# Performance work log

Hardware: AMD Instinct MI355X
Metric: run time of the kernel (lower is better)

The kernel has to match this reference:

```python
import jax, jax.numpy as jnp
import numpy as np

N_NODES = 50000
N_EDGES = 800000
IN_F = 64
D_ATT = 64
HEADS = 8
D_HEAD = D_ATT // HEADS  # 8


def segment_softmax(logits, seg, num_segments):
    # logits: [E, d]; seg: [E] int segment ids
    m = jax.ops.segment_max(logits, seg, num_segments=num_segments)  # [N, d]
    m = jnp.where(jnp.isfinite(m), m, 0.0)  # guard empty segments
    e = jnp.exp(logits - m[seg])
    s = jax.ops.segment_sum(e, seg, num_segments=num_segments)  # [N, d]
    return e / (s[seg] + 1e-16)


def setup_inputs() -> dict:
    key = jax.random.key(0)
    ks = jax.random.split(key, 8)
    x = jax.random.normal(ks[0], (N_NODES, IN_F), dtype=jnp.float32)
    edge = jax.random.randint(ks[1], (2, N_EDGES), 0, N_NODES, dtype=jnp.int32)
    sc = 1.0 / np.sqrt(IN_F).astype(np.float32)
    Wq = jax.random.normal(ks[2], (IN_F, D_ATT), dtype=jnp.float32) * sc
    Wk = jax.random.normal(ks[3], (IN_F, D_ATT), dtype=jnp.float32) * sc
    Wv = jax.random.normal(ks[4], (IN_F, D_ATT), dtype=jnp.float32) * sc
    bq = jnp.zeros((D_ATT,), jnp.float32)
    bk = jnp.zeros((D_ATT,), jnp.float32)
    bv = jnp.zeros((D_ATT,), jnp.float32)
    return {"x": x, "Wq": Wq, "bq": bq, "Wk": Wk, "bk": bk, "Wv": Wv, "bv": bv, "edge": edge}


def reference(x, Wq, bq, Wk, bk, Wv, bv, edge):
    # Linear projections then split heads: [N, H, D_HEAD]
    q = (x @ Wq + bq).reshape(-1, HEADS, D_HEAD)
    k = (x @ Wk + bk).reshape(-1, HEADS, D_HEAD)
    v = (x @ Wv + bv).reshape(-1, HEADS, D_HEAD)
    src = q[edge[0]]      # [E, H, D_HEAD]
    dst_k = k[edge[1]]    # [E, H, D_HEAD]
    # Faithful to source: sum over dim=1 (the HEAD axis) -> [E, D_HEAD]
    prods = jnp.sum(src * dst_k, axis=1) / np.float32(np.sqrt(D_HEAD))
    # segment softmax grouped by edge[attention_norm_idx] (= edge[1])
    attention = segment_softmax(prods, edge[1], N_NODES)
    return attention, v, prods
```

## Files before the change

kernel.cpp:

```cpp
#include <hip/hip_runtime.h>
#include <hip/hip_bf16.h>

#define N_NODES 50000
#define N_EDGES 800000

typedef __attribute__((ext_vector_type(4))) unsigned int uint4v;

static __device__ __forceinline__ float bfu_lo(unsigned int u) {
    union { unsigned int u; float f; } v; v.u = u << 16; return v.f;
}
static __device__ __forceinline__ float bfu_hi(unsigned int u) {
    union { unsigned int u; float f; } v; v.u = u & 0xffff0000u; return v.f;
}
static __device__ __forceinline__ unsigned short f2bf(float f) {
    union { float f; unsigned int u; } v; v.f = f;
    v.u += 0x7fffu + ((v.u >> 16) & 1u);
    return (unsigned short)(v.u >> 16);
}

__global__ __launch_bounds__(256, 4)
void proj_kernel(const float* __restrict__ x,
                 const float* __restrict__ Wq, const float* __restrict__ bq,
                 const float* __restrict__ Wk, const float* __restrict__ bk,
                 const float* __restrict__ Wv, const float* __restrict__ bv,
                 unsigned short* __restrict__ Qb, unsigned short* __restrict__ Kb,
                 float* __restrict__ V)
{
    __shared__ float xs[64 * 64];
    const int tid  = threadIdx.x;
    const int c    = tid & 63;
    const int w    = tid >> 6;
    const int m    = blockIdx.y;
    const int row0 = blockIdx.x * 64;
    const int nrows = min(64, N_NODES - row0);

    const float* W = (m == 0) ? Wq : (m == 1) ? Wk : Wv;
    const float* b = (m == 0) ? bq : (m == 1) ? bk : bv;
    const int oc = (m == 2) ? c : ((c & 7) * 8 + (c >> 3));
    unsigned short* outb = (m == 0) ? Qb : Kb;

    {
        const float4* xg  = (const float4*)(x + (size_t)row0 * 64);
        float4*       xs4 = (float4*)xs;
        const int nf4 = nrows * 16;
        for (int i = tid; i < nf4; i += 256) xs4[i] = xg[i];
    }
    __syncthreads();

    const float bc = b[c];
    const int r0 = w * 16;

    float acc[16];
#pragma unroll
    for (int i = 0; i < 16; ++i) acc[i] = bc;

    for (int jc = 0; jc < 4; ++jc) {
        float wr[16];
#pragma unroll
        for (int j = 0; j < 16; ++j) wr[j] = W[(jc * 16 + j) * 64 + c];
#pragma unroll
        for (int i = 0; i < 16; ++i) {
            const float4* xr = (const float4*)(xs + (r0 + i) * 64 + jc * 16);
#pragma unroll
            for (int j4 = 0; j4 < 4; ++j4) {
                const float4 xv = xr[j4];
                acc[i] += xv.x * wr[4 * j4 + 0];
                acc[i] += xv.y * wr[4 * j4 + 1];
                acc[i] += xv.z * wr[4 * j4 + 2];
                acc[i] += xv.w * wr[4 * j4 + 3];
            }
        }
    }

#pragma unroll
    for (int i = 0; i < 16; ++i) {
        const int r = r0 + i;
        if (r < nrows) {
            const size_t o = (size_t)(row0 + r) * 64 + oc;
            if (m == 2) V[o] = acc[i];
            else        outb[o] = f2bf(acc[i]);
        }
    }
}

__global__ __launch_bounds__(256)
void edge_kernel(const unsigned short* __restrict__ Qb,
                 const unsigned short* __restrict__ Kb,
                 const int* __restrict__ edge,
                 float* __restrict__ prods, float* __restrict__ ssum)
{
    const int gid = blockIdx.x * 256 + threadIdx.x;
    if (gid >= N_EDGES * 8) return;
    const int e = gid >> 3;
    const int d = gid & 7;
    const int e0 = edge[e];
    const int e1 = edge[N_EDGES + e];

    const uint4v qv = *(const uint4v*)(Qb + (size_t)e0 * 64 + d * 8);
    const uint4v kv = *(const uint4v*)(Kb + (size_t)e1 * 64 + d * 8);
    float s = 0.f;
#pragma unroll
    for (int i = 0; i < 4; ++i) {
        s += bfu_lo(qv[i]) * bfu_lo(kv[i]);
        s += bfu_hi(qv[i]) * bfu_hi(kv[i]);
    }

    const float p = s * 0.35355339059327373f;
    prods[gid] = p;
    atomicAdd(ssum + (size_t)e1 * 8 + d, __expf(p));
}

__global__ __launch_bounds__(256)
void norm_kernel(const int* __restrict__ edge,
                 const float* __restrict__ prods,
                 const float* __restrict__ ssum, float* __restrict__ att)
{
    const int gid = blockIdx.x * 256 + threadIdx.x;
    if (gid >= N_EDGES * 8) return;
    const int e = gid >> 3;
    const int d = gid & 7;
    const int e1 = edge[N_EDGES + e];
    const float ex = __expf(prods[gid]);
    att[gid] = ex / (ssum[(size_t)e1 * 8 + d] + 1e-16f);
}

extern "C" void kernel_launch(void* const* d_in, const int* in_sizes, int n_in,
                              void* d_out, int out_size, void* d_ws, size_t ws_size,
                              hipStream_t stream)
{
    const float* x    = (const float*)d_in[0];
    const float* Wq   = (const float*)d_in[1];
    const float* bq   = (const float*)d_in[2];
    const float* Wk   = (const float*)d_in[3];
    const float* bk   = (const float*)d_in[4];
    const float* Wv   = (const float*)d_in[5];
    const float* bv   = (const float*)d_in[6];
    const int*   edge = (const int*)d_in[7];

    float* out   = (float*)d_out;
    float* att   = out;
    float* V     = out + 6400000;
    float* prods = out + 9600000;

    unsigned short* Qb = (unsigned short*)d_ws;
    unsigned short* Kb = Qb + 3200000;
    float*          ssum = (float*)(Kb + 3200000);

    hipMemsetAsync(ssum, 0, 400000 * sizeof(float), stream);

    dim3 pgrid((N_NODES + 63) / 64, 3);
    proj_kernel<<<pgrid, 256, 0, stream>>>(x, Wq, bq, Wk, bk, Wv, bv,
                                           Qb, Kb, V);

    const int nwork = N_EDGES * 8;
    edge_kernel<<<(nwork + 255) / 256, 256, 0, stream>>>(Qb, Kb, edge, prods,
                                                         ssum);
    norm_kernel<<<(nwork + 255) / 256, 256, 0, stream>>>(edge, prods, ssum,
                                                         att);
}
```

Before: 185.9 us.

## Fuse QKV projections into one pass and merge edge/norm via cooperative grid

```diff
diff --git a/kernel.cpp b/kernel.cpp
--- a/kernel.cpp
+++ b/kernel.cpp
@@ -1,8 +1,13 @@
 #include <hip/hip_runtime.h>
 #include <hip/hip_bf16.h>
+#include <hip/hip_cooperative_groups.h>
+
+namespace cg = cooperative_groups;
 
 #define N_NODES 50000
 #define N_EDGES 800000
+
+#define FUSED_THREADS (1024 * 256)
 
 typedef __attribute__((ext_vector_type(4))) unsigned int uint4v;
 
@@ -18,26 +23,20 @@
     return (unsigned short)(v.u >> 16);
 }
 
-__global__ __launch_bounds__(256, 4)
-void proj_kernel(const float* __restrict__ x,
-                 const float* __restrict__ Wq, const float* __restrict__ bq,
-                 const float* __restrict__ Wk, const float* __restrict__ bk,
-                 const float* __restrict__ Wv, const float* __restrict__ bv,
-                 unsigned short* __restrict__ Qb, unsigned short* __restrict__ Kb,
-                 float* __restrict__ V)
+__global__ __launch_bounds__(256, 2)
+void proj_qkv(const float* __restrict__ x,
+              const float* __restrict__ Wq, const float* __restrict__ bq,
+              const float* __restrict__ Wk, const float* __restrict__ bk,
+              const float* __restrict__ Wv, const float* __restrict__ bv,
+              unsigned short* __restrict__ Qb, unsigned short* __restrict__ Kb,
+              float* __restrict__ V)
 {
     __shared__ float xs[64 * 64];
     const int tid  = threadIdx.x;
     const int c    = tid & 63;
     const int w    = tid >> 6;
-    const int m    = blockIdx.y;
     const int row0 = blockIdx.x * 64;
     const int nrows = min(64, N_NODES - row0);
-
-    const float* W = (m == 0) ? Wq : (m == 1) ? Wk : Wv;
-    const float* b = (m == 0) ? bq : (m == 1) ? bk : bv;
-    const int oc = (m == 2) ? c : ((c & 7) * 8 + (c >> 3));
-    unsigned short* outb = (m == 0) ? Qb : Kb;
 
     {
         const float4* xg  = (const float4*)(x + (size_t)row0 * 64);
@@ -47,27 +46,36 @@
     }
     __syncthreads();
 
-    const float bc = b[c];
+    const float* Ws[3] = {Wq, Wk, Wv};
+    const float* bs[3] = {bq, bk, bv};
     const int r0 = w * 16;
+    const int ocqk = (c & 7) * 8 + (c >> 3);
 
-    float acc[16];
+    float acc[3][16];
 #pragma unroll
-    for (int i = 0; i < 16; ++i) acc[i] = bc;
+    for (int m = 0; m < 3; ++m) {
+        const float bc = bs[m][c];
+#pragma unroll
+        for (int i = 0; i < 16; ++i) acc[m][i] = bc;
+    }
 
     for (int jc = 0; jc < 4; ++jc) {
-        float wr[16];
 #pragma unroll
-        for (int j = 0; j < 16; ++j) wr[j] = W[(jc * 16 + j) * 64 + c];
+        for (int m = 0; m < 3; ++m) {
+            float wr[16];
 #pragma unroll
-        for (int i = 0; i < 16; ++i) {
-            const float4* xr = (const float4*)(xs + (r0 + i) * 64 + jc * 16);
+            for (int j = 0; j < 16; ++j) wr[j] = Ws[m][(jc * 16 + j) * 64 + c];
 #pragma unroll
-            for (int j4 = 0; j4 < 4; ++j4) {
-                const float4 xv = xr[j4];
-                acc[i] += xv.x * wr[4 * j4 + 0];
-                acc[i] += xv.y * wr[4 * j4 + 1];
-                acc[i] += xv.z * wr[4 * j4 + 2];
-                acc[i] += xv.w * wr[4 * j4 + 3];
+            for (int i = 0; i < 16; ++i) {
+                const float4* xr = (const float4*)(xs + (r0 + i) * 64 + jc * 16);
+#pragma unroll
+                for (int j4 = 0; j4 < 4; ++j4) {
+                    const float4 xv = xr[j4];
+                    acc[m][i] += xv.x * wr[4 * j4 + 0];
+                    acc[m][i] += xv.y * wr[4 * j4 + 1];
+                    acc[m][i] += xv.z * wr[4 * j4 + 2];
+                    acc[m][i] += xv.w * wr[4 * j4 + 3];
+                }
             }
         }
     }
@@ -76,52 +84,60 @@
     for (int i = 0; i < 16; ++i) {
         const int r = r0 + i;
         if (r < nrows) {
-            const size_t o = (size_t)(row0 + r) * 64 + oc;
-            if (m == 2) V[o] = acc[i];
-            else        outb[o] = f2bf(acc[i]);
+            const size_t o = (size_t)(row0 + r) * 64;
+            Qb[o + ocqk] = f2bf(acc[0][i]);
+            Kb[o + ocqk] = f2bf(acc[1][i]);
+            __builtin_nontemporal_store(acc[2][i], V + o + c);
         }
     }
 }
 
-__global__ __launch_bounds__(256)
-void edge_kernel(const unsigned short* __restrict__ Qb,
-                 const unsigned short* __restrict__ Kb,
-                 const int* __restrict__ edge,
-                 float* __restrict__ prods, float* __restrict__ ssum)
+__global__ __launch_bounds__(256, 4)
+void edge_fused(const unsigned short* __restrict__ Qb,
+                const unsigned short* __restrict__ Kb,
+                const int* __restrict__ edge,
+                float* __restrict__ prods, float* __restrict__ att,
+                float* __restrict__ ssum)
 {
-    const int gid = blockIdx.x * 256 + threadIdx.x;
-    if (gid >= N_EDGES * 8) return;
-    const int e = gid >> 3;
-    const int d = gid & 7;
-    const int e0 = edge[e];
-    const int e1 = edge[N_EDGES + e];
+    const int tid0 = blockIdx.x * 256 + threadIdx.x;
 
-    const uint4v qv = *(const uint4v*)(Qb + (size_t)e0 * 64 + d * 8);
-    const uint4v kv = *(const uint4v*)(Kb + (size_t)e1 * 64 + d * 8);
-    float s = 0.f;
+    for (int i = tid0; i < N_NODES * 8; i += FUSED_THREADS)
+        __hip_atomic_store(ssum + i, 0.f, __ATOMIC_RELAXED,
+                           __HIP_MEMORY_SCOPE_AGENT);
+    __threadfence();
+    cg::this_grid().sync();
+
+    for (int gid = tid0; gid < N_EDGES * 8; gid += FUSED_THREADS) {
+        const int e = gid >> 3;
+        const int d = gid & 7;
+        const int e0 = edge[e];
+        const int e1 = edge[N_EDGES + e];
+
+        const uint4v qv = *(const uint4v*)(Qb + (size_t)e0 * 64 + d * 8);
+        const uint4v kv = *(const uint4v*)(Kb + (size_t)e1 * 64 + d * 8);
+        float s = 0.f;
 #pragma unroll
-    for (int i = 0; i < 4; ++i) {
-        s += bfu_lo(qv[i]) * bfu_lo(kv[i]);
-        s += bfu_hi(qv[i]) * bfu_hi(kv[i]);
+        for (int i = 0; i < 4; ++i) {
+            s += bfu_lo(qv[i]) * bfu_lo(kv[i]);
+            s += bfu_hi(qv[i]) * bfu_hi(kv[i]);
+        }
+        const float p = s * 0.35355339059327373f;
+        prods[gid] = p;
+        atomicAdd(ssum + (size_t)e1 * 8 + d, __expf(p));
     }
+    __threadfence();
+    cg::this_grid().sync();
 
-    const float p = s * 0.35355339059327373f;
-    prods[gid] = p;
-    atomicAdd(ssum + (size_t)e1 * 8 + d, __expf(p));
-}
-
-__global__ __launch_bounds__(256)
-void norm_kernel(const int* __restrict__ edge,
-                 const float* __restrict__ prods,
-                 const float* __restrict__ ssum, float* __restrict__ att)
-{
-    const int gid = blockIdx.x * 256 + threadIdx.x;
-    if (gid >= N_EDGES * 8) return;
-    const int e = gid >> 3;
-    const int d = gid & 7;
-    const int e1 = edge[N_EDGES + e];
-    const float ex = __expf(prods[gid]);
-    att[gid] = ex / (ssum[(size_t)e1 * 8 + d] + 1e-16f);
+    for (int gid = tid0; gid < N_EDGES * 8; gid += FUSED_THREADS) {
+        const int e = gid >> 3;
+        const int d = gid & 7;
+        const int e1 = edge[N_EDGES + e];
+        const float p = prods[gid];
+        const float s = __hip_atomic_load(ssum + (size_t)e1 * 8 + d,
+                                          __ATOMIC_RELAXED,
+                                          __HIP_MEMORY_SCOPE_AGENT);
+        __builtin_nontemporal_store(__expf(p) / (s + 1e-16f), att + gid);
+    }
 }
 
 extern "C" void kernel_launch(void* const* d_in, const int* in_sizes, int n_in,
@@ -146,15 +162,11 @@
     unsigned short* Kb = Qb + 3200000;
     float*          ssum = (float*)(Kb + 3200000);
 
-    hipMemsetAsync(ssum, 0, 400000 * sizeof(float), stream);
+    proj_qkv<<<(N_NODES + 63) / 64, 256, 0, stream>>>(x, Wq, bq, Wk, bk,
+                                                      Wv, bv, Qb, Kb, V);
 
-    dim3 pgrid((N_NODES + 63) / 64, 3);
-    proj_kernel<<<pgrid, 256, 0, stream>>>(x, Wq, bq, Wk, bk, Wv, bv,
-                                           Qb, Kb, V);
-
-    const int nwork = N_EDGES * 8;
-    edge_kernel<<<(nwork + 255) / 256, 256, 0, stream>>>(Qb, Kb, edge, prods,
-                                                         ssum);
-    norm_kernel<<<(nwork + 255) / 256, 256, 0, stream>>>(edge, prods, ssum,
-                                                         att);
+    void* args[] = {(void*)&Qb, (void*)&Kb, (void*)&edge,
+                    (void*)&prods, (void*)&att, (void*)&ssum};
+    hipLaunchCooperativeKernel((void*)edge_fused, dim3(1024), dim3(256),
+                               args, 0, stream);
 }
```

New measurement: 573.7 us. 209% more time.

## Fuse QKV projections into one kernel and fold ssum zeroing in

Applied to the files above, without the earlier changes.

```diff
diff --git a/kernel.cpp b/kernel.cpp
--- a/kernel.cpp
+++ b/kernel.cpp
@@ -18,26 +18,25 @@
     return (unsigned short)(v.u >> 16);
 }
 
-__global__ __launch_bounds__(256, 4)
-void proj_kernel(const float* __restrict__ x,
-                 const float* __restrict__ Wq, const float* __restrict__ bq,
-                 const float* __restrict__ Wk, const float* __restrict__ bk,
-                 const float* __restrict__ Wv, const float* __restrict__ bv,
-                 unsigned short* __restrict__ Qb, unsigned short* __restrict__ Kb,
-                 float* __restrict__ V)
+__global__ __launch_bounds__(256, 2)
+void proj_qkv(const float* __restrict__ x,
+              const float* __restrict__ Wq, const float* __restrict__ bq,
+              const float* __restrict__ Wk, const float* __restrict__ bk,
+              const float* __restrict__ Wv, const float* __restrict__ bv,
+              unsigned short* __restrict__ Qb, unsigned short* __restrict__ Kb,
+              float* __restrict__ V, float* __restrict__ ssum)
 {
-    __shared__ float xs[64 * 64];
+    __shared__ float xs[32 * 64];
     const int tid  = threadIdx.x;
     const int c    = tid & 63;
     const int w    = tid >> 6;
-    const int m    = blockIdx.y;
-    const int row0 = blockIdx.x * 64;
-    const int nrows = min(64, N_NODES - row0);
+    const int row0 = blockIdx.x * 32;
+    const int nrows = min(32, N_NODES - row0);
 
-    const float* W = (m == 0) ? Wq : (m == 1) ? Wk : Wv;
-    const float* b = (m == 0) ? bq : (m == 1) ? bk : bv;
-    const int oc = (m == 2) ? c : ((c & 7) * 8 + (c >> 3));
-    unsigned short* outb = (m == 0) ? Qb : Kb;
+    {
+        const int z = blockIdx.x * 256 + tid;
+        if (z < N_NODES * 8) ssum[z] = 0.f;
+    }
 
     {
         const float4* xg  = (const float4*)(x + (size_t)row0 * 64);
@@ -47,38 +46,44 @@
     }
     __syncthreads();
 
-    const float bc = b[c];
-    const int r0 = w * 16;
+    const int r0 = w * 8;
 
-    float acc[16];
+    float accq[8], acck[8], accv[8];
+    {
+        const float bqc = bq[c], bkc = bk[c], bvc = bv[c];
 #pragma unroll
-    for (int i = 0; i < 16; ++i) acc[i] = bc;
+        for (int i = 0; i < 8; ++i) { accq[i] = bqc; acck[i] = bkc; accv[i] = bvc; }
+    }
 
-    for (int jc = 0; jc < 4; ++jc) {
-        float wr[16];
+    for (int jc = 0; jc < 8; ++jc) {
+        float wq[8], wk[8], wv[8];
 #pragma unroll
-        for (int j = 0; j < 16; ++j) wr[j] = W[(jc * 16 + j) * 64 + c];
+        for (int j = 0; j < 8; ++j) {
+            const int row = (jc * 8 + j) * 64 + c;
+            wq[j] = Wq[row]; wk[j] = Wk[row]; wv[j] = Wv[row];
+        }
 #pragma unroll
-        for (int i = 0; i < 16; ++i) {
-            const float4* xr = (const float4*)(xs + (r0 + i) * 64 + jc * 16);
-#pragma unroll
-            for (int j4 = 0; j4 < 4; ++j4) {
-                const float4 xv = xr[j4];
-                acc[i] += xv.x * wr[4 * j4 + 0];
-                acc[i] += xv.y * wr[4 * j4 + 1];
-                acc[i] += xv.z * wr[4 * j4 + 2];
-                acc[i] += xv.w * wr[4 * j4 + 3];
-            }
+        for (int i = 0; i < 8; ++i) {
+            const float4* xr = (const float4*)(xs + (r0 + i) * 64 + jc * 8);
+            const float4 xv0 = xr[0], xv1 = xr[1];
+            accq[i] += xv0.x * wq[0] + xv0.y * wq[1] + xv0.z * wq[2] + xv0.w * wq[3]
+                     + xv1.x * wq[4] + xv1.y * wq[5] + xv1.z * wq[6] + xv1.w * wq[7];
+            acck[i] += xv0.x * wk[0] + xv0.y * wk[1] + xv0.z * wk[2] + xv0.w * wk[3]
+                     + xv1.x * wk[4] + xv1.y * wk[5] + xv1.z * wk[6] + xv1.w * wk[7];
+            accv[i] += xv0.x * wv[0] + xv0.y * wv[1] + xv0.z * wv[2] + xv0.w * wv[3]
+                     + xv1.x * wv[4] + xv1.y * wv[5] + xv1.z * wv[6] + xv1.w * wv[7];
         }
     }
 
+    const int ocqk = (c & 7) * 8 + (c >> 3);
 #pragma unroll
-    for (int i = 0; i < 16; ++i) {
+    for (int i = 0; i < 8; ++i) {
         const int r = r0 + i;
         if (r < nrows) {
-            const size_t o = (size_t)(row0 + r) * 64 + oc;
-            if (m == 2) V[o] = acc[i];
-            else        outb[o] = f2bf(acc[i]);
+            const size_t o = (size_t)(row0 + r) * 64;
+            Qb[o + ocqk] = f2bf(accq[i]);
+            Kb[o + ocqk] = f2bf(acck[i]);
+            __builtin_nontemporal_store(accv[i], V + o + c);
         }
     }
 }
@@ -121,7 +126,8 @@
     const int d = gid & 7;
     const int e1 = edge[N_EDGES + e];
     const float ex = __expf(prods[gid]);
-    att[gid] = ex / (ssum[(size_t)e1 * 8 + d] + 1e-16f);
+    __builtin_nontemporal_store(ex / (ssum[(size_t)e1 * 8 + d] + 1e-16f),
+                                att + gid);
 }
 
 extern "C" void kernel_launch(void* const* d_in, const int* in_sizes, int n_in,
@@ -146,11 +152,8 @@
     unsigned short* Kb = Qb + 3200000;
     float*          ssum = (float*)(Kb + 3200000);
 
-    hipMemsetAsync(ssum, 0, 400000 * sizeof(float), stream);
-
-    dim3 pgrid((N_NODES + 63) / 64, 3);
-    proj_kernel<<<pgrid, 256, 0, stream>>>(x, Wq, bq, Wk, bk, Wv, bv,
-                                           Qb, Kb, V);
+    proj_qkv<<<(N_NODES + 31) / 32, 256, 0, stream>>>(x, Wq, bq, Wk, bk,
+                                                      Wv, bv, Qb, Kb, V, ssum);
 
     const int nwork = N_EDGES * 8;
     edge_kernel<<<(nwork + 255) / 256, 256, 0, stream>>>(Qb, Kb, edge, prods,
```

After: 176.0 us. 1.06x faster.
